# Kernel optimization log

Measured on AMD Instinct MI355X. Metric: run time of the kernel, lower is better.

The kernel has to match this reference:

```python
import jax, jax.numpy as jnp
import numpy as np

KSIZE = 13
PAD = KSIZE // 2
EPS = 1e-5
MIN_DISP = 1e-3  # clamp to avoid inf depth at zero disparity


def _unfold(x):
    # B,C,H,W -> B, C*k*k, H, W  (im2col with 'same' padding, stride 1; matches F.unfold)
    return jax.lax.conv_general_dilated_patches(
        x, filter_shape=(KSIZE, KSIZE), window_strides=(1, 1),
        padding=[(PAD, PAD), (PAD, PAD)])


def _znorm(p):
    # zero-mean, unit-norm over patch dim -> ZNCC becomes a plain dot product
    p = p - p.mean(axis=1, keepdims=True)
    return p / (jnp.linalg.norm(p, axis=1, keepdims=True) + EPS)


def setup_inputs() -> dict:
    key = jax.random.key(0)
    k1, k2 = jax.random.split(key)
    B, C, H, W = 1, 3, 192, 320
    l_image = jax.random.uniform(k1, (B, C, H, W), jnp.float32)
    # right image = horizontally shifted left + small noise so true matches exist
    r_image = jnp.roll(l_image, shift=-8, axis=-1) + 0.01 * jax.random.normal(k2, (B, C, H, W), jnp.float32)
    fx = 240.0
    intri = jnp.array([[[fx, 0.0, W / 2.0], [0.0, fx, H / 2.0], [0.0, 0.0, 1.0]]], jnp.float32)
    l_extri = jnp.eye(4, dtype=jnp.float32)[None]
    r_extri = l_extri.at[:, 0, 3].set(0.54)  # 0.54 m stereo baseline
    return {"l_image": l_image, "r_image": r_image, "l_intri": intri,
            "r_intri": intri, "l_extri": l_extri, "r_extri": r_extri}


def reference(l_image, r_image, l_intri, r_intri, l_extri, r_extri):
    B, C, H, W = l_image.shape
    # patch unfold (im2col) + ZNCC normalization
    ln = _znorm(_unfold(l_image).reshape(1, -1, H, W))  # 1,D,H,W
    rn = _znorm(_unfold(r_image).reshape(1, -1, H, W))
    # full-width correlation volume: each left pixel vs every right column in its row
    vol = jnp.einsum('bdhw,bdhv->bhwv', ln, rn)  # 1,H,W,W
    # reduce=True -> best-matching right column index
    corresp = jnp.argmax(vol, axis=-1).astype(l_image.dtype)  # 1,H,W
    disp = jnp.abs(corresp - jnp.arange(W, dtype=l_image.dtype))
    # disparity -> depth: depth = fx * baseline / disp
    fx = l_intri[:, 0, 0]
    rel = r_extri @ jnp.linalg.inv(l_extri)  # relative right<-left transform
    baseline = jnp.linalg.norm(rel[:, :3, 3], axis=-1)
    depth = fx[:, None, None] * baseline[:, None, None] / jnp.clip(disp, MIN_DISP, None)
    return depth
```

## Files before the change

kernel.cpp:

```cpp
#include <hip/hip_runtime.h>
#include <math.h>

#define HH 192
#define WW 320
#define DTOT 507.0f
#define KD 39
#define NSPAN 5
#define NCHUNK 5
#define XS 64
#define TV 64
#define TX 76
#define TU 80
#define TUW 76
#define TIS 76
#define TDIAG 77
#define NPIX (HH*WW)

__global__ void prep_kernel(const float* __restrict__ li, const float* __restrict__ le,
                            const float* __restrict__ re, float* __restrict__ sc,
                            unsigned long long* __restrict__ keys) {
    int t = blockIdx.x * blockDim.x + threadIdx.x;
    if (keys != nullptr && t < NPIX) keys[t] = 0ull;
    if (t == 0) {
        float a[4][4], inv[4][4];
        for (int i = 0; i < 4; ++i)
            for (int j = 0; j < 4; ++j) { a[i][j] = le[i*4+j]; inv[i][j] = (i == j) ? 1.0f : 0.0f; }
        for (int c = 0; c < 4; ++c) {
            int p = c; float mx = fabsf(a[c][c]);
            for (int r = c+1; r < 4; ++r) { float v = fabsf(a[r][c]); if (v > mx) { mx = v; p = r; } }
            if (p != c) for (int j = 0; j < 4; ++j) {
                float tq = a[c][j]; a[c][j] = a[p][j]; a[p][j] = tq;
                tq = inv[c][j]; inv[c][j] = inv[p][j]; inv[p][j] = tq;
            }
            float id = 1.0f / a[c][c];
            for (int j = 0; j < 4; ++j) { a[c][j] *= id; inv[c][j] *= id; }
            for (int r = 0; r < 4; ++r) if (r != c) {
                float f = a[r][c];
                for (int j = 0; j < 4; ++j) { a[r][j] -= f*a[c][j]; inv[r][j] -= f*inv[c][j]; }
            }
        }
        float rel[3];
        for (int i = 0; i < 3; ++i)
            rel[i] = re[i*4+0]*inv[0][3] + re[i*4+1]*inv[1][3] + re[i*4+2]*inv[2][3] + re[i*4+3]*inv[3][3];
        float baseline = sqrtf(rel[0]*rel[0] + rel[1]*rel[1] + rel[2]*rel[2]);
        sc[0] = li[0] * baseline;
    }
}

__global__ __launch_bounds__(256) void match_kernel(
        const float* __restrict__ limg, const float* __restrict__ rimg,
        unsigned long long* __restrict__ keys) {
    __shared__ float Ls[KD][TX];
    __shared__ float Rs[KD][TU];
    __shared__ float Tc[TU][TIS];
    __shared__ float colL[TX];
    __shared__ float colR1[TUW];
    __shared__ float colR2[TUW];
    __shared__ float smuR[TV];
    __shared__ float sivR[TV];
    __shared__ float redS[4][XS];
    __shared__ int   redV[4][XS];

    const int span = blockIdx.x;
    const int h    = blockIdx.y;
    const int ch   = blockIdx.z;
    const int wlo  = span * XS;
    const int ulo  = ch * TV;
    const int tid  = threadIdx.x;
    const int lane = tid & 63;
    const int wave = tid >> 6;

    for (int i = tid; i < KD*TX; i += 256) {
        int k = i / TX, xl = i - k*TX;
        int c = k / 13, dy = k - c*13;
        int y = h - 6 + dy, x = wlo - 6 + xl;
        float v = 0.0f;
        if ((unsigned)y < (unsigned)HH && (unsigned)x < (unsigned)WW) v = limg[(c*HH + y)*WW + x];
        Ls[k][xl] = v;
    }
    for (int i = tid; i < KD*TU; i += 256) {
        int k = i / TU, uc = i - k*TU;
        int c = k / 13, dy = k - c*13;
        int y = h - 6 + dy, u = ulo - 6 + uc;
        float v = 0.0f;
        if ((unsigned)y < (unsigned)HH && (unsigned)u < (unsigned)WW) v = rimg[(c*HH + y)*WW + u];
        Rs[k][uc] = v;
    }
    __syncthreads();

    if (tid < TX) {
        float s = 0.0f;
        for (int k = 0; k < KD; ++k) s += Ls[k][tid];
        colL[tid] = s;
    } else if (tid >= 128 && tid < 128 + TUW) {
        int c = tid - 128;
        float s1 = 0.0f, s2 = 0.0f;
        for (int k = 0; k < KD; ++k) {
            float v = Rs[k][c];
            s1 += v;
            s2 = fmaf(v, v, s2);
        }
        colR1[c] = s1;
        colR2[c] = s2;
    }
    __syncthreads();

    float muL;
    {
        float s = 0.0f;
        #pragma unroll
        for (int dx = 0; dx < 13; ++dx) s += colL[lane + dx];
        muL = s / DTOT;
    }

    if (tid < 190) {
        const int ti = tid % 19, tj = tid / 19;
        const int i0 = ti * 4, j0 = tj * 8;
        float a[4][8];
        #pragma unroll
        for (int r = 0; r < 4; ++r)
            #pragma unroll
            for (int c = 0; c < 8; ++c) a[r][c] = 0.0f;
        for (int k = 0; k < KD; ++k) {
            float4 la = *(const float4*)&Ls[k][i0];
            float4 r0 = *(const float4*)&Rs[k][j0];
            float4 r1 = *(const float4*)&Rs[k][j0+4];
            float lx[4] = {la.x, la.y, la.z, la.w};
            float rx[8] = {r0.x, r0.y, r0.z, r0.w, r1.x, r1.y, r1.z, r1.w};
            #pragma unroll
            for (int r = 0; r < 4; ++r)
                #pragma unroll
                for (int c = 0; c < 8; ++c)
                    a[r][c] = fmaf(lx[r], rx[c], a[r][c]);
        }
        #pragma unroll
        for (int c = 0; c < 8; ++c) {
            *(float4*)&Tc[j0+c][i0] = make_float4(a[0][c], a[1][c], a[2][c], a[3][c]);
        }
    } else if (tid >= 192) {
        int vcc = tid - 192;
        float s1 = 0.0f, s2 = 0.0f;
        #pragma unroll
        for (int dx = 0; dx < 13; ++dx) { s1 += colR1[vcc + dx]; s2 += colR2[vcc + dx]; }
        float mu = s1 / DTOT;
        float var = fmaxf(s2 - s1*s1/DTOT, 0.0f);
        smuR[vcc] = mu;
        sivR[vcc] = 1.0f / (sqrtf(var) + 1e-5f);
    }
    __syncthreads();

    float best = -1e30f;
    int bestv = 0;
    const float dml = DTOT * muL;
    for (int vi = 0; vi < 16; ++vi) {
        int vc = wave * 16 + vi;
        const float* tp0 = &Tc[vc][0] + lane;
        float S = 0.0f;
        int boff = 0;
        #pragma unroll
        for (int g = 0; g < 3; ++g) {
            asm volatile("" : "+v"(boff));
            float y0 = tp0[boff];
            float y1 = tp0[boff + TDIAG];
            float y2 = tp0[boff + 2*TDIAG];
            float y3 = tp0[boff + 3*TDIAG];
            S += y0; S += y1; S += y2; S += y3;
            boff += 4*TDIAG;
        }
        S += tp0[12*TDIAG];
        float score = (S - dml * smuR[vc]) * sivR[vc];
        int v = ulo + vc;
        if (score > best) { best = score; bestv = v; }
    }

    redS[wave][lane] = best;
    redV[wave][lane] = bestv;
    __syncthreads();
    if (tid < XS) {
        float b = redS[0][tid]; int bv = redV[0][tid];
        for (int wv = 1; wv < 4; ++wv) {
            float s = redS[wv][tid]; int v2 = redV[wv][tid];
            if (s > b || (s == b && v2 < bv)) { b = s; bv = v2; }
        }
        unsigned ob = __float_as_uint(b);
        ob = (ob & 0x80000000u) ? ~ob : (ob | 0x80000000u);
        unsigned long long key = ((unsigned long long)ob << 32) | (unsigned)(~(unsigned)bv);
        atomicMax(&keys[h*WW + wlo + tid], key);
    }
}

__global__ __launch_bounds__(256) void depth_kernel(const unsigned long long* __restrict__ keys,
                                                    const float* __restrict__ sc,
                                                    float* __restrict__ out) {
    int t = blockIdx.x * 256 + threadIdx.x;
    unsigned long long k = keys[t];
    int v = (int)(~(unsigned int)k);
    float w = (float)(t % WW);
    float disp = fabsf((float)v - w);
    disp = fmaxf(disp, 0.001f);
    out[t] = sc[0] / disp;
}

__global__ __launch_bounds__(256) void match_fallback(
        const float* __restrict__ limg, const float* __restrict__ rimg,
        const float* __restrict__ ws, float* __restrict__ out) {
    __shared__ float Ls[KD][76];
    __shared__ float Rs[KD][76];
    __shared__ float Tt[76][81];
    __shared__ float colL[76];
    __shared__ float colR1[76];
    __shared__ float colR2[76];
    __shared__ float smuR[64];
    __shared__ float sivR[64];
    __shared__ float redS[4][64];
    __shared__ int   redV[4][64];

    const int span = blockIdx.x;
    const int h    = blockIdx.y;
    const int wlo  = span * 64;
    const int tid  = threadIdx.x;
    const int lane = tid & 63;
    const int wave = tid >> 6;

    for (int i = tid; i < KD*76; i += 256) {
        int k = i / 76, xl = i % 76;
        int c = k / 13, dy = k % 13;
        int y = h - 6 + dy, x = wlo - 6 + xl;
        float v = 0.0f;
        if (y >= 0 && y < HH && x >= 0 && x < WW) v = limg[(c*HH + y)*WW + x];
        Ls[k][xl] = v;
    }
    __syncthreads();

    if (tid < 76) {
        float s = 0.0f;
        for (int k = 0; k < KD; ++k) s += Ls[k][tid];
        colL[tid] = s;
    }
    __syncthreads();

    float muL;
    {
        float s = 0.0f;
        #pragma unroll
        for (int dx = 0; dx < 13; ++dx) s += colL[lane + dx];
        muL = s / DTOT;
    }

    float best = -1e30f;
    int bestv = 0;

    for (int ch = 0; ch < NCHUNK; ++ch) {
        const int ulo = ch * 64;
        for (int i = tid; i < KD*76; i += 256) {
            int k = i / 76, uc = i % 76;
            int c = k / 13, dy = k % 13;
            int y = h - 6 + dy, u = ulo - 6 + uc;
            float v = 0.0f;
            if (y >= 0 && y < HH && u >= 0 && u < WW) v = rimg[(c*HH + y)*WW + u];
            Rs[k][uc] = v;
        }
        __syncthreads();

        if (tid < 76) {
            float s1 = 0.0f, s2 = 0.0f;
            for (int k = 0; k < KD; ++k) {
                float v = Rs[k][tid];
                s1 += v;
                s2 = fmaf(v, v, s2);
            }
            colR1[tid] = s1;
            colR2[tid] = s2;
        }

        for (int t = tid; t < 361; t += 256) {
            int ti = t % 19, tj = t / 19;
            int i0 = ti * 4, j0 = tj * 4;
            float a00=0,a01=0,a02=0,a03=0, a10=0,a11=0,a12=0,a13=0;
            float a20=0,a21=0,a22=0,a23=0, a30=0,a31=0,a32=0,a33=0;
            for (int k = 0; k < KD; ++k) {
                float4 la = *(const float4*)&Ls[k][i0];
                float4 rb = *(const float4*)&Rs[k][j0];
                a00 = fmaf(la.x, rb.x, a00); a01 = fmaf(la.x, rb.y, a01);
                a02 = fmaf(la.x, rb.z, a02); a03 = fmaf(la.x, rb.w, a03);
                a10 = fmaf(la.y, rb.x, a10); a11 = fmaf(la.y, rb.y, a11);
                a12 = fmaf(la.y, rb.z, a12); a13 = fmaf(la.y, rb.w, a13);
                a20 = fmaf(la.z, rb.x, a20); a21 = fmaf(la.z, rb.y, a21);
                a22 = fmaf(la.z, rb.z, a22); a23 = fmaf(la.z, rb.w, a23);
                a30 = fmaf(la.w, rb.x, a30); a31 = fmaf(la.w, rb.y, a31);
                a32 = fmaf(la.w, rb.z, a32); a33 = fmaf(la.w, rb.w, a33);
            }
            float* tr0 = &Tt[i0+0][j0]; tr0[0]=a00; tr0[1]=a01; tr0[2]=a02; tr0[3]=a03;
            float* tr1 = &Tt[i0+1][j0]; tr1[0]=a10; tr1[1]=a11; tr1[2]=a12; tr1[3]=a13;
            float* tr2 = &Tt[i0+2][j0]; tr2[0]=a20; tr2[1]=a21; tr2[2]=a22; tr2[3]=a23;
            float* tr3 = &Tt[i0+3][j0]; tr3[0]=a30; tr3[1]=a31; tr3[2]=a32; tr3[3]=a33;
        }
        __syncthreads();

        if (tid < 64) {
            float s1 = 0.0f, s2 = 0.0f;
            #pragma unroll
            for (int dx = 0; dx < 13; ++dx) { s1 += colR1[tid + dx]; s2 += colR2[tid + dx]; }
            float mu = s1 / DTOT;
            float var = fmaxf(s2 - s1*s1/DTOT, 0.0f);
            smuR[tid] = mu;
            sivR[tid] = 1.0f / (sqrtf(var) + 1e-5f);
        }
        __syncthreads();

        for (int vi = 0; vi < 16; ++vi) {
            int vc = wave * 16 + vi;
            int v  = ulo + vc;
            const float* tp = &Tt[lane][vc];
            float S = 0.0f;
            #pragma unroll
            for (int dxp = 0; dxp < 13; ++dxp)
                S += tp[dxp * 82];
            float score = (S - DTOT * muL * smuR[vc]) * sivR[vc];
            if (score > best) { best = score; bestv = v; }
        }
    }

    redS[wave][lane] = best;
    redV[wave][lane] = bestv;
    __syncthreads();
    if (tid < 64) {
        float b = redS[0][tid]; int bv = redV[0][tid];
        for (int wv = 1; wv < 4; ++wv) {
            float s = redS[wv][tid]; int v2 = redV[wv][tid];
            if (s > b || (s == b && v2 < bv)) { b = s; bv = v2; }
        }
        int w = wlo + tid;
        float disp = fabsf((float)bv - (float)w);
        disp = fmaxf(disp, 0.001f);
        out[h*WW + w] = ws[0] / disp;
    }
}

extern "C" void kernel_launch(void* const* d_in, const int* in_sizes, int n_in,
                              void* d_out, int out_size, void* d_ws, size_t ws_size,
                              hipStream_t stream) {
    const float* limg   = (const float*)d_in[0];
    const float* rimg   = (const float*)d_in[1];
    const float* lintri = (const float*)d_in[2];
    const float* lex    = (const float*)d_in[4];
    const float* rex    = (const float*)d_in[5];
    float* out = (float*)d_out;
    float* scp = (float*)d_ws;

    const size_t need = 8 + (size_t)NPIX * 8;
    if (ws_size >= need) {
        unsigned long long* keys = (unsigned long long*)d_ws + 1;
        hipLaunchKernelGGL(prep_kernel, dim3(NPIX/256), dim3(256), 0, stream,
                           lintri, lex, rex, scp, keys);
        hipLaunchKernelGGL(match_kernel, dim3(NSPAN, HH, NCHUNK), dim3(256), 0, stream,
                           limg, rimg, keys);
        hipLaunchKernelGGL(depth_kernel, dim3(NPIX/256), dim3(256), 0, stream,
                           keys, scp, out);
    } else {
        hipLaunchKernelGGL(prep_kernel, dim3(1), dim3(64), 0, stream,
                           lintri, lex, rex, scp, (unsigned long long*)nullptr);
        hipLaunchKernelGGL(match_fallback, dim3(NSPAN, HH), dim3(256), 0, stream,
                           limg, rimg, scp, out);
    }
}
```

Before: 152.1 us.

## Write per-chunk key planes instead of atomics, vectorize tile loads, raise GEMM priority

When the workspace is large enough, each column chunk writes its argmax keys to its own plane and the depth kernel reduces the planes. This removes the 64-bit atomicMax and the separate zeroing of the key buffer in the prep kernel. Global-to-shared tile loads now use float2 accesses with scalar handling at the edges. s_setprio is raised around the FMA inner loop. In exchange the workspace grows to five planes and the depth kernel reads five times as much data.

```diff
diff --git a/kernel.cpp b/kernel.cpp
--- a/kernel.cpp
+++ b/kernel.cpp
@@ -13,7 +13,7 @@
 #define TU 80
 #define TUW 76
 #define TIS 76
-#define TDIAG 77
+#define TD2 77
 #define NPIX (HH*WW)
 
 __global__ void prep_kernel(const float* __restrict__ li, const float* __restrict__ le,
@@ -49,7 +49,7 @@
 
 __global__ __launch_bounds__(256) void match_kernel(
         const float* __restrict__ limg, const float* __restrict__ rimg,
-        unsigned long long* __restrict__ keys) {
+        unsigned long long* __restrict__ sink, int mode) {
     __shared__ float Ls[KD][TX];
     __shared__ float Rs[KD][TU];
     __shared__ float Tc[TU][TIS];
@@ -70,21 +70,37 @@
     const int lane = tid & 63;
     const int wave = tid >> 6;
 
-    for (int i = tid; i < KD*TX; i += 256) {
-        int k = i / TX, xl = i - k*TX;
+    for (int i2 = tid; i2 < KD*38; i2 += 256) {
+        int k = i2 / 38, q = i2 - k*38;
         int c = k / 13, dy = k - c*13;
-        int y = h - 6 + dy, x = wlo - 6 + xl;
-        float v = 0.0f;
-        if ((unsigned)y < (unsigned)HH && (unsigned)x < (unsigned)WW) v = limg[(c*HH + y)*WW + x];
-        Ls[k][xl] = v;
-    }
-    for (int i = tid; i < KD*TU; i += 256) {
-        int k = i / TU, uc = i - k*TU;
+        int y = h - 6 + dy, x0 = wlo - 6 + 2*q;
+        float2 v = make_float2(0.0f, 0.0f);
+        if ((unsigned)y < (unsigned)HH) {
+            const float* row = &limg[(c*HH + y)*WW];
+            if ((unsigned)x0 < (unsigned)(WW-1)) {
+                v = *(const float2*)&row[x0];
+            } else {
+                if ((unsigned)x0 < (unsigned)WW) v.x = row[x0];
+                if ((unsigned)(x0+1) < (unsigned)WW) v.y = row[x0+1];
+            }
+        }
+        *(float2*)&Ls[k][2*q] = v;
+    }
+    for (int i2 = tid; i2 < KD*40; i2 += 256) {
+        int k = i2 / 40, q = i2 - k*40;
         int c = k / 13, dy = k - c*13;
-        int y = h - 6 + dy, u = ulo - 6 + uc;
-        float v = 0.0f;
-        if ((unsigned)y < (unsigned)HH && (unsigned)u < (unsigned)WW) v = rimg[(c*HH + y)*WW + u];
-        Rs[k][uc] = v;
+        int y = h - 6 + dy, u0 = ulo - 6 + 2*q;
+        float2 v = make_float2(0.0f, 0.0f);
+        if ((unsigned)y < (unsigned)HH) {
+            const float* row = &rimg[(c*HH + y)*WW];
+            if ((unsigned)u0 < (unsigned)(WW-1)) {
+                v = *(const float2*)&row[u0];
+            } else {
+                if ((unsigned)u0 < (unsigned)WW) v.x = row[u0];
+                if ((unsigned)(u0+1) < (unsigned)WW) v.y = row[u0+1];
+            }
+        }
+        *(float2*)&Rs[k][2*q] = v;
     }
     __syncthreads();
 
@@ -121,6 +137,7 @@
         for (int r = 0; r < 4; ++r)
             #pragma unroll
             for (int c = 0; c < 8; ++c) a[r][c] = 0.0f;
+        __builtin_amdgcn_s_setprio(1);
         for (int k = 0; k < KD; ++k) {
             float4 la = *(const float4*)&Ls[k][i0];
             float4 r0 = *(const float4*)&Rs[k][j0];
@@ -133,10 +150,10 @@
                 for (int c = 0; c < 8; ++c)
                     a[r][c] = fmaf(lx[r], rx[c], a[r][c]);
         }
-        #pragma unroll
-        for (int c = 0; c < 8; ++c) {
+        __builtin_amdgcn_s_setprio(0);
+        #pragma unroll
+        for (int c = 0; c < 8; ++c)
             *(float4*)&Tc[j0+c][i0] = make_float4(a[0][c], a[1][c], a[2][c], a[3][c]);
-        }
     } else if (tid >= 192) {
         int vcc = tid - 192;
         float s1 = 0.0f, s2 = 0.0f;
@@ -161,13 +178,13 @@
         for (int g = 0; g < 3; ++g) {
             asm volatile("" : "+v"(boff));
             float y0 = tp0[boff];
-            float y1 = tp0[boff + TDIAG];
-            float y2 = tp0[boff + 2*TDIAG];
-            float y3 = tp0[boff + 3*TDIAG];
+            float y1 = tp0[boff + TD2];
+            float y2 = tp0[boff + 2*TD2];
+            float y3 = tp0[boff + 3*TD2];
             S += y0; S += y1; S += y2; S += y3;
-            boff += 4*TDIAG;
-        }
-        S += tp0[12*TDIAG];
+            boff += 4*TD2;
+        }
+        S += tp0[12*TD2];
         float score = (S - dml * smuR[vc]) * sivR[vc];
         int v = ulo + vc;
         if (score > best) { best = score; bestv = v; }
@@ -185,19 +202,29 @@
         unsigned ob = __float_as_uint(b);
         ob = (ob & 0x80000000u) ? ~ob : (ob | 0x80000000u);
         unsigned long long key = ((unsigned long long)ob << 32) | (unsigned)(~(unsigned)bv);
-        atomicMax(&keys[h*WW + wlo + tid], key);
+        if (mode) {
+            sink[(size_t)ch * NPIX + h*WW + wlo + tid] = key;
+        } else {
+            atomicMax(&sink[h*WW + wlo + tid], key);
+        }
     }
 }
 
-__global__ __launch_bounds__(256) void depth_kernel(const unsigned long long* __restrict__ keys,
+__global__ __launch_bounds__(256) void depth_kernel(const unsigned long long* __restrict__ sink,
                                                     const float* __restrict__ sc,
-                                                    float* __restrict__ out) {
+                                                    float* __restrict__ out, int mode) {
     int t = blockIdx.x * 256 + threadIdx.x;
-    unsigned long long k = keys[t];
+    unsigned long long k = sink[t];
+    if (mode) {
+        #pragma unroll
+        for (int p = 1; p < NCHUNK; ++p) {
+            unsigned long long k2 = sink[(size_t)p * NPIX + t];
+            if (k2 > k) k = k2;
+        }
+    }
     int v = (int)(~(unsigned int)k);
     float w = (float)(t % WW);
-    float disp = fabsf((float)v - w);
-    disp = fmaxf(disp, 0.001f);
+    float disp = fmaxf(fabsf((float)v - w), 0.001f);
     out[t] = sc[0] / disp;
 }
 
@@ -348,15 +375,24 @@
     float* out = (float*)d_out;
     float* scp = (float*)d_ws;
 
-    const size_t need = 8 + (size_t)NPIX * 8;
-    if (ws_size >= need) {
+    const size_t needA = 8 + (size_t)NCHUNK * NPIX * 8;
+    const size_t needB = 8 + (size_t)NPIX * 8;
+    if (ws_size >= needA) {
+        unsigned long long* planes = (unsigned long long*)d_ws + 1;
+        hipLaunchKernelGGL(prep_kernel, dim3(1), dim3(64), 0, stream,
+                           lintri, lex, rex, scp, (unsigned long long*)nullptr);
+        hipLaunchKernelGGL(match_kernel, dim3(NSPAN, HH, NCHUNK), dim3(256), 0, stream,
+                           limg, rimg, planes, 1);
+        hipLaunchKernelGGL(depth_kernel, dim3(NPIX/256), dim3(256), 0, stream,
+                           planes, scp, out, 1);
+    } else if (ws_size >= needB) {
         unsigned long long* keys = (unsigned long long*)d_ws + 1;
         hipLaunchKernelGGL(prep_kernel, dim3(NPIX/256), dim3(256), 0, stream,
                            lintri, lex, rex, scp, keys);
         hipLaunchKernelGGL(match_kernel, dim3(NSPAN, HH, NCHUNK), dim3(256), 0, stream,
-                           limg, rimg, keys);
+                           limg, rimg, keys, 0);
         hipLaunchKernelGGL(depth_kernel, dim3(NPIX/256), dim3(256), 0, stream,
-                           keys, scp, out);
+                           keys, scp, out, 0);
     } else {
         hipLaunchKernelGGL(prep_kernel, dim3(1), dim3(64), 0, stream,
                            lintri, lex, rex, scp, (unsigned long long*)nullptr);
```

Result: faster. 142.3 us (-6.5%).
